# Kernel tuning notes

Measured on AMD Instinct MI355X. Metric: run time of the kernel, lower is better.

## Reference

```python
import jax, jax.numpy as jnp
import numpy as np

N = 50000
E = 800000
IN_CH = 128
OUT_CH = 32
HEADS = 2
NEG_SLOPE = 0.2


def setup_inputs() -> dict:
    key = jax.random.key(0)
    k_x, k_ei, k_w, k_as, k_ad, k_b = jax.random.split(key, 6)
    x = jax.random.normal(k_x, (N, IN_CH), dtype=jnp.float32)
    edge_index = jax.random.randint(k_ei, (2, E), 0, N, dtype=jnp.int64)
    # Glorot-style init scale for linear weight and attention vectors
    w_scale = 1.0 / np.sqrt(IN_CH)
    W = jax.random.normal(k_w, (IN_CH, HEADS * OUT_CH), dtype=jnp.float32) * w_scale
    a_scale = 1.0 / np.sqrt(OUT_CH)
    a_src = jax.random.normal(k_as, (HEADS, OUT_CH), dtype=jnp.float32) * a_scale
    a_dst = jax.random.normal(k_ad, (HEADS, OUT_CH), dtype=jnp.float32) * a_scale
    bias = jnp.zeros((HEADS * OUT_CH,), dtype=jnp.float32)
    return {"x": x, "edge_index": edge_index, "W": W, "a_src": a_src,
            "a_dst": a_dst, "bias": bias}


def reference(x, edge_index, W, a_src, a_dst, bias):
    n = x.shape[0]
    # add self-loops (add_self_loops=True); static shape E+N
    loops = jnp.tile(jnp.arange(n, dtype=edge_index.dtype), (2, 1))
    ei = jnp.concatenate([edge_index, loops], axis=1)
    src, dst = ei[0], ei[1]

    # linear projection -> per-head features [N, H, C]
    h = (x @ W).reshape(n, HEADS, OUT_CH)

    # per-node attention logits [N, H]
    alpha_s = jnp.sum(h * a_src[None], axis=-1)
    alpha_d = jnp.sum(h * a_dst[None], axis=-1)

    # per-edge score, LeakyReLU, segment softmax over edges grouped by dst
    e = jax.nn.leaky_relu(alpha_s[src] + alpha_d[dst], NEG_SLOPE)  # [E', H]
    e_max = jax.ops.segment_max(e, dst, num_segments=n)           # [N, H]
    e_exp = jnp.exp(e - e_max[dst])
    denom = jax.ops.segment_sum(e_exp, dst, num_segments=n)       # [N, H]
    alpha = e_exp / (denom[dst] + 1e-16)                          # [E', H]

    # scatter-add weighted messages [N, H, C]
    out = jax.ops.segment_sum(alpha[:, :, None] * h[src], dst, num_segments=n)
    # concat heads + bias (concat=True)
    return out.reshape(n, HEADS * OUT_CH) + bias
```

## Files before the change

kernel.cpp:

```cpp
#include <hip/hip_runtime.h>
#include <hip/hip_bf16.h>
#include <hip/hip_fp16.h>
#include <math.h>

#define IN_CH   128
#define OUT_CH  32
#define HEADS   2
#define HC      (HEADS * OUT_CH)
#define NEG_SLOPE 0.2f

#define NODE_TILE 64
#define X_STRIDE  132

#define BIN_CAP 64

__global__ __launch_bounds__(256) void gemm_alpha_kernel(
    const float* __restrict__ x, const float* __restrict__ W,
    const float* __restrict__ a_src, const float* __restrict__ a_dst,
    __half* __restrict__ h, float* __restrict__ alpha_s, float* __restrict__ alpha_d,
    int* __restrict__ deg, int n_nodes)
{
    __shared__ float Ws[IN_CH * HC];
    __shared__ float Xs[NODE_TILE * X_STRIDE];

    const int tid = threadIdx.x;
    const int node0 = blockIdx.x * NODE_TILE;

    if (tid < NODE_TILE && node0 + tid < n_nodes) deg[node0 + tid] = 0;

    const float4* W4 = (const float4*)W;
    float4* Ws4 = (float4*)Ws;
    #pragma unroll
    for (int i = 0; i < 8; ++i) Ws4[tid + i * 256] = W4[tid + i * 256];

    const float4* X4 = (const float4*)x;
    #pragma unroll
    for (int i = 0; i < 8; ++i) {
        int idx = tid + i * 256;
        int r = idx >> 5, c4 = idx & 31;
        int node = node0 + r;
        float4 v = make_float4(0.f, 0.f, 0.f, 0.f);
        if (node < n_nodes) v = X4[(size_t)node * (IN_CH / 4) + c4];
        *(float4*)&Xs[r * X_STRIDE + c4 * 4] = v;
    }
    __syncthreads();

    const int n    = tid >> 3;
    const int g    = tid & 7;
    const int col0 = g * 8;
    const int head = col0 >> 5;
    const int c0   = col0 & 31;

    float accA[8] = {0,0,0,0,0,0,0,0};
    float accB[8] = {0,0,0,0,0,0,0,0};
    const float* xa = &Xs[n * X_STRIDE];
    const float* xb = &Xs[(n + 32) * X_STRIDE];
    #pragma unroll 8
    for (int k = 0; k < IN_CH; ++k) {
        float va = xa[k], vb = xb[k];
        const float4 w0 = *(const float4*)&Ws[k * HC + col0];
        const float4 w1 = *(const float4*)&Ws[k * HC + col0 + 4];
        accA[0] += va * w0.x; accA[1] += va * w0.y;
        accA[2] += va * w0.z; accA[3] += va * w0.w;
        accA[4] += va * w1.x; accA[5] += va * w1.y;
        accA[6] += va * w1.z; accA[7] += va * w1.w;
        accB[0] += vb * w0.x; accB[1] += vb * w0.y;
        accB[2] += vb * w0.z; accB[3] += vb * w0.w;
        accB[4] += vb * w1.x; accB[5] += vb * w1.y;
        accB[6] += vb * w1.z; accB[7] += vb * w1.w;
    }

    float asr[8], adr[8];
    #pragma unroll
    for (int j = 0; j < 8; ++j) {
        asr[j] = a_src[head * OUT_CH + c0 + j];
        adr[j] = a_dst[head * OUT_CH + c0 + j];
    }

    #pragma unroll
    for (int half = 0; half < 2; ++half) {
        const float* acc = half ? accB : accA;
        const int node = node0 + n + half * 32;
        if (node < n_nodes) {
            unsigned u[8];
            #pragma unroll
            for (int j = 0; j < 8; ++j) u[j] = __half_as_ushort(__float2half_rn(acc[j]));
            int4 v = make_int4((int)(u[0] | (u[1] << 16)), (int)(u[2] | (u[3] << 16)),
                               (int)(u[4] | (u[5] << 16)), (int)(u[6] | (u[7] << 16)));
            *(int4*)&h[(size_t)node * HC + col0] = v;
        }
        float ps = 0.f, pd = 0.f;
        #pragma unroll
        for (int j = 0; j < 8; ++j) { ps += acc[j] * asr[j]; pd += acc[j] * adr[j]; }
        ps += __shfl_xor(ps, 1); ps += __shfl_xor(ps, 2);
        pd += __shfl_xor(pd, 1); pd += __shfl_xor(pd, 2);
        if ((g & 3) == 0 && node < n_nodes) {
            alpha_s[node * HEADS + head] = ps;
            alpha_d[node * HEADS + head] = pd;
        }
    }
}

__global__ void edge_kernel(const int* __restrict__ src, const int* __restrict__ dst,
                            int* __restrict__ deg,
                            const float* __restrict__ alpha_s, const float* __restrict__ alpha_d,
                            int2* __restrict__ bins, int n_edges, int n_total)
{
    int e = blockIdx.x * blockDim.x + threadIdx.x;
    if (e >= n_total) return;
    int s, d;
    if (e < n_edges) { s = src[e]; d = dst[e]; }
    else             { s = d = e - n_edges; }
    float2 as = ((const float2*)alpha_s)[s];
    float2 ad = ((const float2*)alpha_d)[d];
    float v0 = as.x + ad.x;
    float v1 = as.y + ad.y;
    v0 = (v0 > 0.f) ? v0 : NEG_SLOPE * v0;
    v1 = (v1 > 0.f) ? v1 : NEG_SLOPE * v1;
    unsigned u0 = __half_as_ushort(__float2half_rn(__expf(v0)));
    unsigned u1 = __half_as_ushort(__float2half_rn(__expf(v1)));
    int rk = atomicAdd(&deg[d], 1);
    if (rk < BIN_CAP) {
        int2 rec;
        rec.x = s;
        rec.y = (int)((u1 << 16) | u0);
        bins[(size_t)d * BIN_CAP + rk] = rec;
    }
}

__device__ __forceinline__ float unpack_p(int py, int head) {
    unsigned u = (unsigned)py;
    unsigned short us = (unsigned short)(head ? (u >> 16) : (u & 0xffffu));
    return __half2float(__ushort_as_half(us));
}

__global__ __launch_bounds__(256) void node_gather_kernel(
    const int2* __restrict__ bins, const int* __restrict__ deg,
    const __half* __restrict__ h, const float* __restrict__ bias,
    float* __restrict__ out, int n_nodes)
{
    int node = blockIdx.x * (blockDim.x >> 6) + (threadIdx.x >> 6);
    if (node >= n_nodes) return;
    const int lane = threadIdx.x & 63;
    const int head = lane >> 5;
    int cnt = deg[node];
    if (cnt > BIN_CAP) cnt = BIN_CAP;
    const int2* ep = bins + (size_t)node * BIN_CAP;

    int rx = 0, ry = 0;
    if (lane < cnt) { int2 r = ep[lane]; rx = r.x; ry = r.y; }

    float acc = 0.f, lsum = 0.f;
    for (int i = 0; i < cnt; i += 8) {
        #pragma unroll
        for (int j = 0; j < 8; ++j) {
            int idx = i + j;
            int sj = __shfl(rx, idx);
            int yj = __shfl(ry, idx);
            float pj = (idx < cnt) ? unpack_p(yj, head) : 0.f;
            float hj = __half2float(h[(size_t)sj * HC + lane]);
            acc += pj * hj;
            lsum += pj;
        }
    }
    out[(size_t)node * HC + lane] = acc / (lsum + 1e-16f) + bias[lane];
}

extern "C" void kernel_launch(void* const* d_in, const int* in_sizes, int n_in,
                              void* d_out, int out_size, void* d_ws, size_t ws_size,
                              hipStream_t stream)
{
    const float* x      = (const float*)d_in[0];
    const int*   ei     = (const int*)d_in[1];
    const float* W      = (const float*)d_in[2];
    const float* a_src  = (const float*)d_in[3];
    const float* a_dst  = (const float*)d_in[4];
    const float* bias   = (const float*)d_in[5];
    float* out = (float*)d_out;

    const int n_nodes = in_sizes[0] / IN_CH;
    const int n_edges = in_sizes[1] / 2;
    const int n_total = n_edges + n_nodes;

    const int* src = ei;
    const int* dst = ei + n_edges;

    __half* h      = (__half*)d_ws;
    float* alpha_s = (float*)(h + (size_t)n_nodes * HC);
    float* alpha_d = alpha_s + (size_t)n_nodes * HEADS;
    int* deg       = (int*)(alpha_d + (size_t)n_nodes * HEADS);
    uintptr_t ep   = (uintptr_t)(deg + n_nodes);
    ep = (ep + 15) & ~(uintptr_t)15;
    int2* bins     = (int2*)ep;

    const int edge_blocks = (n_total + 255) / 256;
    const int gemm_blocks = (n_nodes + NODE_TILE - 1) / NODE_TILE;

    gemm_alpha_kernel<<<gemm_blocks, 256, 0, stream>>>(
        x, W, a_src, a_dst, h, alpha_s, alpha_d, deg, n_nodes);

    edge_kernel<<<edge_blocks, 256, 0, stream>>>(
        src, dst, deg, alpha_s, alpha_d, bins, n_edges, n_total);

    int ng_blocks = (n_nodes + 3) / 4;
    node_gather_kernel<<<ng_blocks, 256, 0, stream>>>(
        bins, deg, h, bias, out, n_nodes);
}
```

Baseline: 183.2 us.

## Overlap degree histogram atomics with GEMM by merging into one launch

The per-destination atomic rank counting moves out of the edge kernel into extra blocks of the GEMM kernel, so the atomics run concurrently with the projection GEMM. Ranks are stored in a new workspace array and read back by a lighter fill kernel, and deg is zeroed by a memset instead of inside the GEMM. This adds a memset launch and an extra rank write and read per edge. The added blocks also share the device with the shared-memory-heavy GEMM blocks.

```diff
diff --git a/kernel.cpp b/kernel.cpp
--- a/kernel.cpp
+++ b/kernel.cpp
@@ -14,19 +14,28 @@
 
 #define BIN_CAP 64
 
-__global__ __launch_bounds__(256) void gemm_alpha_kernel(
+__global__ __launch_bounds__(256) void gemm_hist_kernel(
     const float* __restrict__ x, const float* __restrict__ W,
     const float* __restrict__ a_src, const float* __restrict__ a_dst,
     __half* __restrict__ h, float* __restrict__ alpha_s, float* __restrict__ alpha_d,
-    int* __restrict__ deg, int n_nodes)
-{
+    const int* __restrict__ dst, int* __restrict__ deg, int* __restrict__ rank,
+    int n_nodes, int n_edges, int n_total, int gemm_blocks)
+{
+    const int tid = threadIdx.x;
+
+    if (blockIdx.x >= gemm_blocks) {
+        int e = (blockIdx.x - gemm_blocks) * blockDim.x + tid;
+        if (e < n_total) {
+            int d = (e < n_edges) ? dst[e] : (e - n_edges);
+            rank[e] = atomicAdd(&deg[d], 1);
+        }
+        return;
+    }
+
     __shared__ float Ws[IN_CH * HC];
     __shared__ float Xs[NODE_TILE * X_STRIDE];
 
-    const int tid = threadIdx.x;
     const int node0 = blockIdx.x * NODE_TILE;
-
-    if (tid < NODE_TILE && node0 + tid < n_nodes) deg[node0 + tid] = 0;
 
     const float4* W4 = (const float4*)W;
     float4* Ws4 = (float4*)Ws;
@@ -101,8 +110,8 @@
     }
 }
 
-__global__ void edge_kernel(const int* __restrict__ src, const int* __restrict__ dst,
-                            int* __restrict__ deg,
+__global__ void fill_kernel(const int* __restrict__ src, const int* __restrict__ dst,
+                            const int* __restrict__ rank,
                             const float* __restrict__ alpha_s, const float* __restrict__ alpha_d,
                             int2* __restrict__ bins, int n_edges, int n_total)
 {
@@ -113,13 +122,13 @@
     else             { s = d = e - n_edges; }
     float2 as = ((const float2*)alpha_s)[s];
     float2 ad = ((const float2*)alpha_d)[d];
+    int rk = rank[e];
     float v0 = as.x + ad.x;
     float v1 = as.y + ad.y;
     v0 = (v0 > 0.f) ? v0 : NEG_SLOPE * v0;
     v1 = (v1 > 0.f) ? v1 : NEG_SLOPE * v1;
     unsigned u0 = __half_as_ushort(__float2half_rn(__expf(v0)));
     unsigned u1 = __half_as_ushort(__float2half_rn(__expf(v1)));
-    int rk = atomicAdd(&deg[d], 1);
     if (rk < BIN_CAP) {
         int2 rec;
         rec.x = s;
@@ -189,18 +198,22 @@
     float* alpha_s = (float*)(h + (size_t)n_nodes * HC);
     float* alpha_d = alpha_s + (size_t)n_nodes * HEADS;
     int* deg       = (int*)(alpha_d + (size_t)n_nodes * HEADS);
-    uintptr_t ep   = (uintptr_t)(deg + n_nodes);
+    int* rank      = deg + n_nodes;
+    uintptr_t ep   = (uintptr_t)(rank + n_total);
     ep = (ep + 15) & ~(uintptr_t)15;
     int2* bins     = (int2*)ep;
 
     const int edge_blocks = (n_total + 255) / 256;
     const int gemm_blocks = (n_nodes + NODE_TILE - 1) / NODE_TILE;
 
-    gemm_alpha_kernel<<<gemm_blocks, 256, 0, stream>>>(
-        x, W, a_src, a_dst, h, alpha_s, alpha_d, deg, n_nodes);
-
-    edge_kernel<<<edge_blocks, 256, 0, stream>>>(
-        src, dst, deg, alpha_s, alpha_d, bins, n_edges, n_total);
+    hipMemsetAsync(deg, 0, (size_t)n_nodes * sizeof(int), stream);
+
+    gemm_hist_kernel<<<gemm_blocks + edge_blocks, 256, 0, stream>>>(
+        x, W, a_src, a_dst, h, alpha_s, alpha_d,
+        dst, deg, rank, n_nodes, n_edges, n_total, gemm_blocks);
+
+    fill_kernel<<<edge_blocks, 256, 0, stream>>>(
+        src, dst, rank, alpha_s, alpha_d, bins, n_edges, n_total);
 
     int ng_blocks = (n_nodes + 3) / 4;
     node_gather_kernel<<<ng_blocks, 256, 0, stream>>>(
```

Measured after the change: 171.2 us. -6.5%, faster.
